# Kernel optimization log

Measured on AMD Instinct MI355X. Metric: run time of the kernel, lower is better.

## Reference

```python
import jax, jax.numpy as jnp
import numpy as np

B, N, C, H, K = 16, 1024, 384, 6, 8
HID = int(C * 2.0)  # mlp_ratio = 2.0
HD = C // H


def _layernorm(x, w, b, eps=1e-5):
    m = x.mean(-1, keepdims=True)
    v = ((x - m) ** 2).mean(-1, keepdims=True)
    return (x - m) * jax.lax.rsqrt(v + eps) * w + b


def setup_inputs() -> dict:
    key = jax.random.key(0)
    ks = jax.random.split(key, 16)
    x = jax.random.normal(ks[0], (B, N, C), jnp.float32)
    # knn indices within each batch, offset by batch*N (as in get_knn_index)
    idx = jax.random.randint(ks[1], (B, K, N), 0, N)
    base = jnp.arange(B, dtype=jnp.int32)[:, None, None] * N
    knn_index = (idx + base).reshape(-1).astype(jnp.int32)
    s = 0.02
    p = {
        "x": x,
        "knn_index": knn_index,
        "ln1_w": jnp.ones((C,), jnp.float32),
        "ln1_b": jnp.zeros((C,), jnp.float32),
        "w_qkv": jax.random.normal(ks[2], (C, 3 * C), jnp.float32) * s,  # qkv_bias=False
        "w_proj": jax.random.normal(ks[3], (C, C), jnp.float32) * s,
        "b_proj": jnp.zeros((C,), jnp.float32),
        "w_knn": jax.random.normal(ks[4], (2 * C, C), jnp.float32) * s,
        "b_knn": jnp.zeros((C,), jnp.float32),
        "w_merge": jax.random.normal(ks[5], (2 * C, C), jnp.float32) * s,
        "b_merge": jnp.zeros((C,), jnp.float32),
        "ln2_w": jnp.ones((C,), jnp.float32),
        "ln2_b": jnp.zeros((C,), jnp.float32),
        "w_fc1": jax.random.normal(ks[6], (C, HID), jnp.float32) * s,
        "b_fc1": jnp.zeros((HID,), jnp.float32),
        "w_fc2": jax.random.normal(ks[7], (HID, C), jnp.float32) * s,
        "b_fc2": jnp.zeros((C,), jnp.float32),
    }
    return p


def reference(x, knn_index, ln1_w, ln1_b, w_qkv, w_proj, b_proj, w_knn, b_knn,
              w_merge, b_merge, ln2_w, ln2_b, w_fc1, b_fc1, w_fc2, b_fc2):
    nx = _layernorm(x, ln1_w, ln1_b)  # [B,N,C]

    # --- self attention ---
    qkv = (nx @ w_qkv).reshape(B, N, 3, H, HD)
    q, k, v = qkv[:, :, 0], qkv[:, :, 1], qkv[:, :, 2]  # [B,N,H,HD]
    scale = HD ** (-0.5)
    attn = jnp.einsum("bnhd,bmhd->bhnm", q, k) * scale
    attn = jax.nn.softmax(attn, axis=-1)
    a_out = jnp.einsum("bhnm,bmhd->bnhd", attn, v).reshape(B, N, C)
    x1 = a_out @ w_proj + b_proj

    # --- graph feature: gather, relative concat, Linear+LeakyReLU, max over k ---
    feat = nx.reshape(B * N, C)[knn_index].reshape(B, K, N, C)
    center = nx[:, None, :, :]  # [B,1,N,C]
    g = jnp.concatenate([feat - center, jnp.broadcast_to(center, (B, K, N, C))], axis=-1)
    knn_f = jax.nn.leaky_relu(g @ w_knn + b_knn, negative_slope=0.2)
    knn_f = knn_f.max(axis=1)  # [B,N,C]

    x1 = jnp.concatenate([x1, knn_f], axis=-1) @ w_merge + b_merge
    x = x + x1

    # --- MLP ---
    h = _layernorm(x, ln2_w, ln2_b)
    h = jax.nn.gelu(h @ w_fc1 + b_fc1, approximate=False) @ w_fc2 + b_fc2
    return x + h
```

## Files before the change

kernel.cpp:

```cpp
#include <hip/hip_runtime.h>
#include <hip/hip_bf16.h>
#include <math.h>

#define BN_ROWS 16384
#define CDIM 384
#define NH 6
#define BBATCH 16
#define NNN 1024

typedef unsigned short u16;
typedef unsigned int u32;
typedef __attribute__((ext_vector_type(8))) short short8;
typedef __attribute__((ext_vector_type(4))) float floatx4;

__device__ __forceinline__ float b2f(u16 s) { return __uint_as_float(((u32)s) << 16); }
__device__ __forceinline__ u16 f2b(float f) {
    __hip_bfloat16 h = __float2bfloat16(f);
    u16 s; __builtin_memcpy(&s, &h, 2); return s;
}
__device__ __forceinline__ void gload_lds16(const u16* g, u16* l) {
    __builtin_amdgcn_global_load_lds(
        (const __attribute__((address_space(1))) unsigned int*)g,
        (__attribute__((address_space(3))) unsigned int*)l, 16, 0, 0);
}

__global__ __launch_bounds__(256) void pack_all(
    const float* __restrict__ W0, u16* __restrict__ T0,
    const float* __restrict__ W1, u16* __restrict__ T1,
    const float* __restrict__ W2, u16* __restrict__ T2,
    const float* __restrict__ W3, u16* __restrict__ T3,
    const float* __restrict__ W4, u16* __restrict__ T4,
    const float* __restrict__ W5, u16* __restrict__ T5)
{
    const float* W; u16* T; int K, N;
    switch (blockIdx.z) {
        case 0: W = W0; T = T0; K = 384; N = 1152; break;
        case 1: W = W1; T = T1; K = 384; N = 384;  break;
        case 2: W = W2; T = T2; K = 768; N = 384;  break;
        case 3: W = W3; T = T3; K = 768; N = 384;  break;
        case 4: W = W4; T = T4; K = 384; N = 768;  break;
        default: W = W5; T = T5; K = 768; N = 384; break;
    }
    const int n0 = blockIdx.x * 32, k0 = blockIdx.y * 32;
    if (n0 >= N || k0 >= K) return;
    __shared__ float s[32][33];
    const int tx = threadIdx.x & 31, ty = threadIdx.x >> 5;
#pragma unroll
    for (int i = 0; i < 4; ++i)
        s[ty + 8 * i][tx] = W[(size_t)(k0 + ty + 8 * i) * N + n0 + tx];
    __syncthreads();
#pragma unroll
    for (int i = 0; i < 4; ++i)
        T[(size_t)(n0 + ty + 8 * i) * K + k0 + tx] = f2b(s[tx][ty + 8 * i]);
}

__global__ __launch_bounds__(64) void ln_kernel(const float* __restrict__ xin,
                                                const float* __restrict__ w,
                                                const float* __restrict__ b,
                                                u16* __restrict__ out)
{
    const int row = blockIdx.x;
    const int t = threadIdx.x;
    const size_t base = (size_t)row * CDIM;
    float v[6];
#pragma unroll
    for (int i = 0; i < 6; ++i) v[i] = xin[base + t + 64 * i];
    float s = 0.f, s2 = 0.f;
#pragma unroll
    for (int i = 0; i < 6; ++i) { s += v[i]; s2 += v[i] * v[i]; }
#pragma unroll
    for (int m = 1; m < 64; m <<= 1) {
        s  += __shfl_xor(s,  m, 64);
        s2 += __shfl_xor(s2, m, 64);
    }
    const float mean = s * (1.0f / CDIM);
    const float var  = s2 * (1.0f / CDIM) - mean * mean;
    const float rs   = rsqrtf(var + 1e-5f);
#pragma unroll
    for (int i = 0; i < 6; ++i) {
        int c = t + 64 * i;
        out[base + c] = f2b((v[i] - mean) * rs * w[c] + b[c]);
    }
}

template<int ACT, bool HAS_BIAS, bool HAS_RES, bool OUT_F32, int MODE>
__global__ __launch_bounds__(256) void gemm_mfma_kernel(
    const u16* __restrict__ A, int lda,
    const u16* __restrict__ Bt, const u16* __restrict__ Bt2, int ldbt,
    u16* Cb, u16* Cb2, float* Cf, int ldc,
    const float* __restrict__ bias,
    const float* res,
    int K)
{
    __shared__ u16 As[128 * 32];
    __shared__ u16 Bs[128 * 32];
    const int tid  = threadIdx.x;
    const int wv   = tid >> 6;
    const int lane = tid & 63;
    const int l15  = lane & 15;
    const int quad = lane >> 4;
    const int m0 = blockIdx.y * 128;
    const int n0 = blockIdx.x * 128;
    const int woffm = (wv >> 1) * 64;
    const int woffn = (wv & 1) * 64;

    const u16* bsrc = (MODE == 2 && n0 >= 384) ? Bt2 : Bt;
    const int  bn0  = (MODE == 2 && n0 >= 384) ? (n0 - 384) : n0;

    floatx4 acc[4][4];
#pragma unroll
    for (int mt = 0; mt < 4; ++mt)
#pragma unroll
        for (int nt = 0; nt < 4; ++nt) acc[mt][nt] = (floatx4){0.f, 0.f, 0.f, 0.f};

    const int gsw  = 8 * ((lane & 3) ^ ((lane >> 3) & 3));
    const int rloc = lane >> 2;
    const int rdsw = 8 * (quad ^ ((l15 >> 1) & 3));

    for (int kt = 0; kt < K; kt += 32) {
#pragma unroll
        for (int j = 0; j < 2; ++j) {
            const int slab = 32 * wv + 16 * j;
            const int r = slab + rloc;
            gload_lds16(A    + (size_t)(m0  + r) * lda  + kt + gsw, &As[slab * 32]);
            gload_lds16(bsrc + (size_t)(bn0 + r) * ldbt + kt + gsw, &Bs[slab * 32]);
        }
        __syncthreads();

        short8 af[4], bf[4];
#pragma unroll
        for (int mt = 0; mt < 4; ++mt)
            af[mt] = *(const short8*)(As + (woffm + mt * 16 + l15) * 32 + rdsw);
#pragma unroll
        for (int nt = 0; nt < 4; ++nt)
            bf[nt] = *(const short8*)(Bs + (woffn + nt * 16 + l15) * 32 + rdsw);
#pragma unroll
        for (int mt = 0; mt < 4; ++mt)
#pragma unroll
            for (int nt = 0; nt < 4; ++nt)
                acc[mt][nt] = __builtin_amdgcn_mfma_f32_16x16x32_bf16(
                    af[mt], bf[nt], acc[mt][nt], 0, 0, 0);
        __syncthreads();
    }

#pragma unroll
    for (int nt = 0; nt < 4; ++nt) {
        const int gc = n0 + woffn + nt * 16 + l15;
        float bi = 0.f;
        if (HAS_BIAS) bi = bias[gc];
        if (MODE == 2) bi = (gc >= 384) ? bias[gc - 384] : 0.f;
#pragma unroll
        for (int mt = 0; mt < 4; ++mt) {
            const int gr0 = m0 + woffm + mt * 16 + quad * 4;
#pragma unroll
            for (int rr = 0; rr < 4; ++rr) {
                float v = acc[mt][nt][rr] + bi;
                if (ACT == 1) v = 0.5f * v * (1.0f + erff(v * 0.70710678118654752f));
                if (HAS_RES)  v += res[(size_t)(gr0 + rr) * ldc + gc];
                if (MODE == 1) {
                    const int t3  = gc / 384;
                    const int rem = gc - t3 * 384;
                    const int hh = rem >> 6, dd = rem & 63;
                    const int bb = (gr0 + rr) >> 10, nn = (gr0 + rr) & 1023;
                    Cb[((size_t)((bb * 6 + hh) * 1024 + nn)) * 192 + t3 * 64 + dd] = f2b(v);
                } else if (MODE == 2) {
                    if (gc < 384) Cb [(size_t)(gr0 + rr) * 384 + gc]       = f2b(v);
                    else          Cb2[(size_t)(gr0 + rr) * 384 + gc - 384] = f2b(v);
                } else if (OUT_F32) {
                    Cf[(size_t)(gr0 + rr) * ldc + gc] = v;
                } else {
                    Cb[(size_t)(gr0 + rr) * ldc + gc] = f2b(v);
                }
            }
        }
    }
}

__global__ __launch_bounds__(256) void attn_mfma_kernel(const u16* __restrict__ qkv2,
                                                        u16* __restrict__ aout)
{
    const int id = blockIdx.x;
    const int rxcd = id & 7;
    const int j = id >> 3;
    const int slab = rxcd + 8 * (j % 12);
    const int qtile = j / 12;
    const int b = slab / NH, h = slab % NH;

    const int wave = threadIdx.x >> 6;
    const int lane = threadIdx.x & 63;
    const int l15 = lane & 15;
    const int quad = lane >> 4;
    const int qbase = qtile * 128 + wave * 32;
    const int tid = threadIdx.x;

    const u16* slabp = qkv2 + ((size_t)(b * NH + h) << 10) * 192;

    __shared__ u16 Ks[64 * 72];
    __shared__ u16 Vt[64 * 72];
    __shared__ u16 Ps[4][32 * 72];

    short8 qf[2][2];
#pragma unroll
    for (int mt = 0; mt < 2; ++mt) {
        const u16* qrow = slabp + (size_t)(qbase + mt * 16 + l15) * 192;
        qf[mt][0] = *(const short8*)(qrow + quad * 8);
        qf[mt][1] = *(const short8*)(qrow + 32 + quad * 8);
    }

    float rowsum[2][4];
    floatx4 Oacc[2][4];
#pragma unroll
    for (int mt = 0; mt < 2; ++mt)
#pragma unroll
        for (int nt = 0; nt < 4; ++nt) {
            Oacc[mt][nt] = (floatx4){0.f, 0.f, 0.f, 0.f};
            rowsum[mt][nt] = 0.f;
        }

    for (int kc = 0; kc < NNN; kc += 64) {
        {
            const int key = tid >> 2, dblk = (tid & 3) * 16;
            const u16* kp = slabp + (size_t)(kc + key) * 192 + 64 + dblk;
            *(short8*)(Ks + key * 72 + dblk)     = *(const short8*)(kp);
            *(short8*)(Ks + key * 72 + dblk + 8) = *(const short8*)(kp + 8);
        }
        {
            const int kp2 = tid & 31, db = (tid >> 5) * 8;
            const u16* v0p = slabp + (size_t)(kc + 2 * kp2) * 192 + 128 + db;
            uint4 v0 = *(const uint4*)(v0p);
            uint4 v1 = *(const uint4*)(v0p + 192);
            u32 a0[4] = {v0.x, v0.y, v0.z, v0.w};
            u32 a1[4] = {v1.x, v1.y, v1.z, v1.w};
#pragma unroll
            for (int i = 0; i < 8; ++i) {
                u32 w0 = (i & 1) ? (a0[i >> 1] >> 16) : (a0[i >> 1] & 0xffffu);
                u32 w1 = (i & 1) ? (a1[i >> 1] >> 16) : (a1[i >> 1] & 0xffffu);
                *(u32*)(Vt + (size_t)(db + i) * 72 + 2 * kp2) = w0 | (w1 << 16);
            }
        }
        __syncthreads();

        floatx4 sc[2][4];
#pragma unroll
        for (int nt = 0; nt < 4; ++nt) {
            short8 kf0 = *(const short8*)(Ks + (nt * 16 + l15) * 72 + quad * 8);
            short8 kf1 = *(const short8*)(Ks + (nt * 16 + l15) * 72 + 32 + quad * 8);
#pragma unroll
            for (int mt = 0; mt < 2; ++mt) {
                floatx4 s = {0.f, 0.f, 0.f, 0.f};
                s = __builtin_amdgcn_mfma_f32_16x16x32_bf16(qf[mt][0], kf0, s, 0, 0, 0);
                s = __builtin_amdgcn_mfma_f32_16x16x32_bf16(qf[mt][1], kf1, s, 0, 0, 0);
                sc[mt][nt] = s;
            }
        }

#pragma unroll
        for (int mt = 0; mt < 2; ++mt)
#pragma unroll
            for (int nt = 0; nt < 4; ++nt)
#pragma unroll
                for (int rr = 0; rr < 4; ++rr) {
                    float p = __expf(sc[mt][nt][rr] * 0.125f);
                    rowsum[mt][rr] += p;
                    Ps[wave][(mt * 16 + quad * 4 + rr) * 72 + nt * 16 + l15] = f2b(p);
                }

        short8 pf[2][2];
#pragma unroll
        for (int mt = 0; mt < 2; ++mt) {
            pf[mt][0] = *(const short8*)(Ps[wave] + (mt * 16 + l15) * 72 + quad * 8);
            pf[mt][1] = *(const short8*)(Ps[wave] + (mt * 16 + l15) * 72 + 32 + quad * 8);
        }

#pragma unroll
        for (int nt = 0; nt < 4; ++nt) {
#pragma unroll
            for (int kk = 0; kk < 2; ++kk) {
                short8 vf = *(const short8*)(Vt + (size_t)(nt * 16 + l15) * 72 + kk * 32 + quad * 8);
#pragma unroll
                for (int mt = 0; mt < 2; ++mt)
                    Oacc[mt][nt] = __builtin_amdgcn_mfma_f32_16x16x32_bf16(
                        pf[mt][kk], vf, Oacc[mt][nt], 0, 0, 0);
            }
        }
        __syncthreads();
    }

#pragma unroll
    for (int mt = 0; mt < 2; ++mt)
#pragma unroll
        for (int rr = 0; rr < 4; ++rr) {
            float l = rowsum[mt][rr];
#pragma unroll
            for (int m = 1; m < 16; m <<= 1) l += __shfl_xor(l, m, 64);
            float inv = 1.0f / l;
            int q = qbase + mt * 16 + quad * 4 + rr;
#pragma unroll
            for (int nt = 0; nt < 4; ++nt)
                aout[(size_t)(b * NNN + q) * CDIM + h * 64 + nt * 16 + l15] =
                    f2b(Oacc[mt][nt][rr] * inv);
        }
}

__global__ __launch_bounds__(128) void knnmax_kernel(const u16* __restrict__ t1,
                                                     const u16* __restrict__ t2,
                                                     const int* __restrict__ idx,
                                                     u16* __restrict__ x1cat)
{
    const int bn = blockIdx.x;
    const int b = bn >> 10, n = bn & 1023;
    int ind[8];
#pragma unroll
    for (int k = 0; k < 8; ++k) ind[k] = idx[b * 8192 + k * 1024 + n];
    const size_t rbase = (size_t)bn * CDIM;
    for (int c = threadIdx.x; c < CDIM; c += 128) {
        float base = b2f(t2[rbase + c]) - b2f(t1[rbase + c]);
        float mx = -1e30f;
#pragma unroll
        for (int k = 0; k < 8; ++k) {
            float v = b2f(t1[(size_t)ind[k] * CDIM + c]) + base;
            v = (v > 0.f) ? v : 0.2f * v;
            mx = fmaxf(mx, v);
        }
        x1cat[(size_t)bn * 768 + CDIM + c] = f2b(mx);
    }
}

extern "C" void kernel_launch(void* const* d_in, const int* in_sizes, int n_in,
                              void* d_out, int out_size, void* d_ws, size_t ws_size,
                              hipStream_t stream)
{
    (void)in_sizes; (void)n_in; (void)out_size; (void)ws_size;
    const float* x     = (const float*)d_in[0];
    const int*   knn   = (const int*)d_in[1];
    const float* ln1w  = (const float*)d_in[2];
    const float* ln1b  = (const float*)d_in[3];
    const float* wqkv  = (const float*)d_in[4];
    const float* wproj = (const float*)d_in[5];
    const float* bproj = (const float*)d_in[6];
    const float* wknn  = (const float*)d_in[7];
    const float* bknn  = (const float*)d_in[8];
    const float* wmrg  = (const float*)d_in[9];
    const float* bmrg  = (const float*)d_in[10];
    const float* ln2w  = (const float*)d_in[11];
    const float* ln2b  = (const float*)d_in[12];
    const float* wfc1  = (const float*)d_in[13];
    const float* bfc1  = (const float*)d_in[14];
    const float* wfc2  = (const float*)d_in[15];
    const float* bfc2  = (const float*)d_in[16];

    u16* wsb = (u16*)d_ws;
    const size_t RE = (size_t)BN_ROWS * CDIM;
    u16* nxb   = wsb;
    u16* qkvb  = wsb + RE;
    u16* x1cat = wsb + RE;
    u16* t1b   = wsb + 3 * RE;
    u16* hinb  = wsb;
    u16* h1b   = wsb + RE;
    u16* wqkvT  = wsb + 4 * RE;
    u16* wprojT = wqkvT + 442368;
    u16* wknnT  = wprojT + 147456;
    u16* wmrgT  = wknnT + 294912;
    u16* wfc1T  = wmrgT + 294912;
    u16* wfc2T  = wfc1T + 294912;
    u16*   aoutb = (u16*)d_out;
    u16*   t2b   = (u16*)d_out;
    float* xmid  = (float*)d_out;

    pack_all<<<dim3(36, 24, 6), 256, 0, stream>>>(
        wqkv, wqkvT, wproj, wprojT, wknn, wknnT, wmrg, wmrgT, wfc1, wfc1T, wfc2, wfc2T);
    ln_kernel<<<BN_ROWS, 64, 0, stream>>>(x, ln1w, ln1b, nxb);
    gemm_mfma_kernel<0, false, false, false, 1><<<dim3(9, 128), 256, 0, stream>>>(
        nxb, CDIM, wqkvT, nullptr, CDIM, qkvb, nullptr, nullptr, 0, nullptr, nullptr, CDIM);
    attn_mfma_kernel<<<768, 256, 0, stream>>>(qkvb, aoutb);
    gemm_mfma_kernel<0, true, false, false, 0><<<dim3(3, 128), 256, 0, stream>>>(
        aoutb, CDIM, wprojT, nullptr, CDIM, x1cat, nullptr, nullptr, 768, bproj, nullptr, CDIM);
    gemm_mfma_kernel<0, false, false, false, 2><<<dim3(6, 128), 256, 0, stream>>>(
        nxb, CDIM, wknnT, wknnT + 384, 768, t1b, t2b, nullptr, CDIM, bknn, nullptr, CDIM);
    knnmax_kernel<<<BN_ROWS, 128, 0, stream>>>(t1b, t2b, knn, x1cat);
    gemm_mfma_kernel<0, true, true, true, 0><<<dim3(3, 128), 256, 0, stream>>>(
        x1cat, 768, wmrgT, nullptr, 768, nullptr, nullptr, xmid, CDIM, bmrg, x, 768);
    ln_kernel<<<BN_ROWS, 64, 0, stream>>>(xmid, ln2w, ln2b, hinb);
    gemm_mfma_kernel<1, true, false, false, 0><<<dim3(6, 128), 256, 0, stream>>>(
        hinb, CDIM, wfc1T, nullptr, CDIM, h1b, nullptr, nullptr, 768, bfc1, nullptr, CDIM);
    gemm_mfma_kernel<0, true, true, true, 0><<<dim3(3, 128), 256, 0, stream>>>(
        h1b, 768, wfc2T, nullptr, 768, nullptr, nullptr, (float*)d_out, CDIM, bfc2, xmid, 768);
}
```

Baseline: 357.1 us.

## Use 64-wide N tiles for narrow GEMMs and transpose score MFMA in attention

The GEMM kernel gains an NT template parameter, and the three GEMMs with 384 output columns use 128x64 tiles, doubling their grid from 384 to 768 blocks to fill more compute units. In the attention kernel the score MFMA swaps operands to produce S^T, so each lane packs four bf16 probabilities into a single 8-byte LDS store instead of four scalar stores. The softmax row sums then need only two shuffles plus a small LDS exchange instead of a 4-step shuffle reduction. Smaller N tiles reduce A-tile reuse per block, which costs extra global load traffic.

```diff
diff --git a/kernel.cpp b/kernel.cpp
--- a/kernel.cpp
+++ b/kernel.cpp
@@ -83,7 +83,7 @@
     }
 }
 
-template<int ACT, bool HAS_BIAS, bool HAS_RES, bool OUT_F32, int MODE>
+template<int ACT, bool HAS_BIAS, bool HAS_RES, bool OUT_F32, int MODE, int NT>
 __global__ __launch_bounds__(256) void gemm_mfma_kernel(
     const u16* __restrict__ A, int lda,
     const u16* __restrict__ Bt, const u16* __restrict__ Bt2, int ldbt,
@@ -92,26 +92,27 @@
     const float* res,
     int K)
 {
+    constexpr int NTL = NT / 32;
     __shared__ u16 As[128 * 32];
-    __shared__ u16 Bs[128 * 32];
+    __shared__ u16 Bs[NT * 32];
     const int tid  = threadIdx.x;
     const int wv   = tid >> 6;
     const int lane = tid & 63;
     const int l15  = lane & 15;
     const int quad = lane >> 4;
     const int m0 = blockIdx.y * 128;
-    const int n0 = blockIdx.x * 128;
+    const int n0 = blockIdx.x * NT;
     const int woffm = (wv >> 1) * 64;
-    const int woffn = (wv & 1) * 64;
+    const int woffn = (wv & 1) * (NT / 2);
 
     const u16* bsrc = (MODE == 2 && n0 >= 384) ? Bt2 : Bt;
     const int  bn0  = (MODE == 2 && n0 >= 384) ? (n0 - 384) : n0;
 
-    floatx4 acc[4][4];
+    floatx4 acc[4][NTL];
 #pragma unroll
     for (int mt = 0; mt < 4; ++mt)
 #pragma unroll
-        for (int nt = 0; nt < 4; ++nt) acc[mt][nt] = (floatx4){0.f, 0.f, 0.f, 0.f};
+        for (int nt = 0; nt < NTL; ++nt) acc[mt][nt] = (floatx4){0.f, 0.f, 0.f, 0.f};
 
     const int gsw  = 8 * ((lane & 3) ^ ((lane >> 3) & 3));
     const int rloc = lane >> 2;
@@ -121,30 +122,38 @@
 #pragma unroll
         for (int j = 0; j < 2; ++j) {
             const int slab = 32 * wv + 16 * j;
-            const int r = slab + rloc;
-            gload_lds16(A    + (size_t)(m0  + r) * lda  + kt + gsw, &As[slab * 32]);
-            gload_lds16(bsrc + (size_t)(bn0 + r) * ldbt + kt + gsw, &Bs[slab * 32]);
+            gload_lds16(A + (size_t)(m0 + slab + rloc) * lda + kt + gsw, &As[slab * 32]);
+        }
+        if (NT == 128) {
+#pragma unroll
+            for (int j = 0; j < 2; ++j) {
+                const int slab = 32 * wv + 16 * j;
+                gload_lds16(bsrc + (size_t)(bn0 + slab + rloc) * ldbt + kt + gsw, &Bs[slab * 32]);
+            }
+        } else {
+            const int slab = 16 * wv;
+            gload_lds16(bsrc + (size_t)(bn0 + slab + rloc) * ldbt + kt + gsw, &Bs[slab * 32]);
         }
         __syncthreads();
 
-        short8 af[4], bf[4];
+        short8 af[4], bf[NTL];
 #pragma unroll
         for (int mt = 0; mt < 4; ++mt)
             af[mt] = *(const short8*)(As + (woffm + mt * 16 + l15) * 32 + rdsw);
 #pragma unroll
-        for (int nt = 0; nt < 4; ++nt)
+        for (int nt = 0; nt < NTL; ++nt)
             bf[nt] = *(const short8*)(Bs + (woffn + nt * 16 + l15) * 32 + rdsw);
 #pragma unroll
         for (int mt = 0; mt < 4; ++mt)
 #pragma unroll
-            for (int nt = 0; nt < 4; ++nt)
+            for (int nt = 0; nt < NTL; ++nt)
                 acc[mt][nt] = __builtin_amdgcn_mfma_f32_16x16x32_bf16(
                     af[mt], bf[nt], acc[mt][nt], 0, 0, 0);
         __syncthreads();
     }
 
 #pragma unroll
-    for (int nt = 0; nt < 4; ++nt) {
+    for (int nt = 0; nt < NTL; ++nt) {
         const int gc = n0 + woffn + nt * 16 + l15;
         float bi = 0.f;
         if (HAS_BIAS) bi = bias[gc];
@@ -195,27 +204,25 @@
 
     const u16* slabp = qkv2 + ((size_t)(b * NH + h) << 10) * 192;
 
-    __shared__ u16 Ks[64 * 72];
-    __shared__ u16 Vt[64 * 72];
-    __shared__ u16 Ps[4][32 * 72];
+    __shared__ __align__(16) u16 Ks[64 * 72];
+    __shared__ __align__(16) u16 Vt[64 * 72];
+    __shared__ __align__(16) u16 Ps[4][32 * 72];
+    __shared__ __align__(16) float Ls[4][32];
 
     short8 qf[2][2];
 #pragma unroll
-    for (int mt = 0; mt < 2; ++mt) {
-        const u16* qrow = slabp + (size_t)(qbase + mt * 16 + l15) * 192;
-        qf[mt][0] = *(const short8*)(qrow + quad * 8);
-        qf[mt][1] = *(const short8*)(qrow + 32 + quad * 8);
-    }
-
-    float rowsum[2][4];
+    for (int nt = 0; nt < 2; ++nt) {
+        const u16* qrow = slabp + (size_t)(qbase + nt * 16 + l15) * 192;
+        qf[nt][0] = *(const short8*)(qrow + quad * 8);
+        qf[nt][1] = *(const short8*)(qrow + 32 + quad * 8);
+    }
+
+    float rowsum[2] = {0.f, 0.f};
     floatx4 Oacc[2][4];
 #pragma unroll
     for (int mt = 0; mt < 2; ++mt)
 #pragma unroll
-        for (int nt = 0; nt < 4; ++nt) {
-            Oacc[mt][nt] = (floatx4){0.f, 0.f, 0.f, 0.f};
-            rowsum[mt][nt] = 0.f;
-        }
+        for (int nt = 0; nt < 4; ++nt) Oacc[mt][nt] = (floatx4){0.f, 0.f, 0.f, 0.f};
 
     for (int kc = 0; kc < NNN; kc += 64) {
         {
@@ -240,30 +247,36 @@
         }
         __syncthreads();
 
-        floatx4 sc[2][4];
-#pragma unroll
-        for (int nt = 0; nt < 4; ++nt) {
-            short8 kf0 = *(const short8*)(Ks + (nt * 16 + l15) * 72 + quad * 8);
-            short8 kf1 = *(const short8*)(Ks + (nt * 16 + l15) * 72 + 32 + quad * 8);
-#pragma unroll
-            for (int mt = 0; mt < 2; ++mt) {
+        floatx4 sc[4][2];
+#pragma unroll
+        for (int kt_ = 0; kt_ < 4; ++kt_) {
+            short8 kf0 = *(const short8*)(Ks + (kt_ * 16 + l15) * 72 + quad * 8);
+            short8 kf1 = *(const short8*)(Ks + (kt_ * 16 + l15) * 72 + 32 + quad * 8);
+#pragma unroll
+            for (int nt = 0; nt < 2; ++nt) {
                 floatx4 s = {0.f, 0.f, 0.f, 0.f};
-                s = __builtin_amdgcn_mfma_f32_16x16x32_bf16(qf[mt][0], kf0, s, 0, 0, 0);
-                s = __builtin_amdgcn_mfma_f32_16x16x32_bf16(qf[mt][1], kf1, s, 0, 0, 0);
-                sc[mt][nt] = s;
-            }
-        }
-
-#pragma unroll
-        for (int mt = 0; mt < 2; ++mt)
-#pragma unroll
-            for (int nt = 0; nt < 4; ++nt)
+                s = __builtin_amdgcn_mfma_f32_16x16x32_bf16(kf0, qf[nt][0], s, 0, 0, 0);
+                s = __builtin_amdgcn_mfma_f32_16x16x32_bf16(kf1, qf[nt][1], s, 0, 0, 0);
+                sc[kt_][nt] = s;
+            }
+        }
+
+#pragma unroll
+        for (int kt_ = 0; kt_ < 4; ++kt_)
+#pragma unroll
+            for (int nt = 0; nt < 2; ++nt) {
+                u16 pk[4];
 #pragma unroll
                 for (int rr = 0; rr < 4; ++rr) {
-                    float p = __expf(sc[mt][nt][rr] * 0.125f);
-                    rowsum[mt][rr] += p;
-                    Ps[wave][(mt * 16 + quad * 4 + rr) * 72 + nt * 16 + l15] = f2b(p);
+                    float p = __expf(sc[kt_][nt][rr] * 0.125f);
+                    rowsum[nt] += p;
+                    pk[rr] = f2b(p);
                 }
+                u32 lo = (u32)pk[0] | ((u32)pk[1] << 16);
+                u32 hi = (u32)pk[2] | ((u32)pk[3] << 16);
+                *(uint2*)(Ps[wave] + (nt * 16 + l15) * 72 + kt_ * 16 + quad * 4) =
+                    make_uint2(lo, hi);
+            }
 
         short8 pf[2][2];
 #pragma unroll
@@ -271,7 +284,6 @@
             pf[mt][0] = *(const short8*)(Ps[wave] + (mt * 16 + l15) * 72 + quad * 8);
             pf[mt][1] = *(const short8*)(Ps[wave] + (mt * 16 + l15) * 72 + 32 + quad * 8);
         }
-
 #pragma unroll
         for (int nt = 0; nt < 4; ++nt) {
 #pragma unroll
@@ -287,19 +299,26 @@
     }
 
 #pragma unroll
-    for (int mt = 0; mt < 2; ++mt)
+    for (int nt = 0; nt < 2; ++nt) {
+        float l = rowsum[nt];
+        l += __shfl_xor(l, 16, 64);
+        l += __shfl_xor(l, 32, 64);
+        if (quad == 0) Ls[wave][nt * 16 + l15] = l;
+    }
+#pragma unroll
+    for (int mt = 0; mt < 2; ++mt) {
+        float4 lv = *(const float4*)&Ls[wave][mt * 16 + quad * 4];
+        float li[4] = {lv.x, lv.y, lv.z, lv.w};
 #pragma unroll
         for (int rr = 0; rr < 4; ++rr) {
-            float l = rowsum[mt][rr];
-#pragma unroll
-            for (int m = 1; m < 16; m <<= 1) l += __shfl_xor(l, m, 64);
-            float inv = 1.0f / l;
+            float inv = 1.0f / li[rr];
             int q = qbase + mt * 16 + quad * 4 + rr;
 #pragma unroll
             for (int nt = 0; nt < 4; ++nt)
                 aout[(size_t)(b * NNN + q) * CDIM + h * 64 + nt * 16 + l15] =
                     f2b(Oacc[mt][nt][rr] * inv);
         }
+    }
 }
 
 __global__ __launch_bounds__(128) void knnmax_kernel(const u16* __restrict__ t1,
@@ -370,19 +389,19 @@
     pack_all<<<dim3(36, 24, 6), 256, 0, stream>>>(
         wqkv, wqkvT, wproj, wprojT, wknn, wknnT, wmrg, wmrgT, wfc1, wfc1T, wfc2, wfc2T);
     ln_kernel<<<BN_ROWS, 64, 0, stream>>>(x, ln1w, ln1b, nxb);
-    gemm_mfma_kernel<0, false, false, false, 1><<<dim3(9, 128), 256, 0, stream>>>(
+    gemm_mfma_kernel<0, false, false, false, 1, 128><<<dim3(9, 128), 256, 0, stream>>>(
         nxb, CDIM, wqkvT, nullptr, CDIM, qkvb, nullptr, nullptr, 0, nullptr, nullptr, CDIM);
     attn_mfma_kernel<<<768, 256, 0, stream>>>(qkvb, aoutb);
-    gemm_mfma_kernel<0, true, false, false, 0><<<dim3(3, 128), 256, 0, stream>>>(
+    gemm_mfma_kernel<0, true, false, false, 0, 64><<<dim3(6, 128), 256, 0, stream>>>(
         aoutb, CDIM, wprojT, nullptr, CDIM, x1cat, nullptr, nullptr, 768, bproj, nullptr, CDIM);
-    gemm_mfma_kernel<0, false, false, false, 2><<<dim3(6, 128), 256, 0, stream>>>(
+    gemm_mfma_kernel<0, false, false, false, 2, 128><<<dim3(6, 128), 256, 0, stream>>>(
         nxb, CDIM, wknnT, wknnT + 384, 768, t1b, t2b, nullptr, CDIM, bknn, nullptr, CDIM);
     knnmax_kernel<<<BN_ROWS, 128, 0, stream>>>(t1b, t2b, knn, x1cat);
-    gemm_mfma_kernel<0, true, true, true, 0><<<dim3(3, 128), 256, 0, stream>>>(
+    gemm_mfma_kernel<0, true, true, true, 0, 64><<<dim3(6, 128), 256, 0, stream>>>(
         x1cat, 768, wmrgT, nullptr, 768, nullptr, nullptr, xmid, CDIM, bmrg, x, 768);
     ln_kernel<<<BN_ROWS, 64, 0, stream>>>(xmid, ln2w, ln2b, hinb);
-    gemm_mfma_kernel<1, true, false, false, 0><<<dim3(6, 128), 256, 0, stream>>>(
+    gemm_mfma_kernel<1, true, false, false, 0, 128><<<dim3(6, 128), 256, 0, stream>>>(
         hinb, CDIM, wfc1T, nullptr, CDIM, h1b, nullptr, nullptr, 768, bfc1, nullptr, CDIM);
-    gemm_mfma_kernel<0, true, true, true, 0><<<dim3(3, 128), 256, 0, stream>>>(
+    gemm_mfma_kernel<0, true, true, true, 0, 64><<<dim3(6, 128), 256, 0, stream>>>(
         h1b, 768, wfc2T, nullptr, 768, nullptr, nullptr, (float*)d_out, CDIM, bfc2, xmid, 768);
 }
```

New measurement: 345.5 us. 1.03x faster.
